# Performance work log

Hardware: AMD Instinct MI355X
Metric: run time of the kernel (lower is better)

## Reference

```python
import jax, jax.numpy as jnp
import numpy as np
from jax import lax

EPS = 1e-8


def _moving_average(x, window):
    # x: [B, T]; replicate-pad left by window-1, then mean-filter (matches F.pad(mode='replicate') + conv1d)
    pad = jnp.repeat(x[:, :1], window - 1, axis=1)
    xp = jnp.concatenate([pad, x], axis=1)[:, None, :]          # [B, 1, T+w-1]
    k = (jnp.ones((1, 1, window), x.dtype) / window)
    out = lax.conv_general_dilated(xp, k, (1,), 'VALID')         # [B, 1, T]
    return out[:, 0, :]


def _ema(x, period):
    # linear recurrence ema[t] = a*x[t] + (1-a)*ema[t-1], ema[0] = x[0]
    alpha = 2.0 / (period + 1)
    def step(carry, xt):
        y = alpha * xt + (1.0 - alpha) * carry
        return y, y
    init = x[:, 0]
    _, ys = lax.scan(step, init, x[:, 1:].T)                     # ys: [T-1, B]
    return jnp.concatenate([x[:, :1], ys.T], axis=1)


def _rsi(close, period=14):
    delta = jnp.diff(close, axis=1, prepend=close[:, :1])
    gain = jnp.where(delta > 0, delta, 0.0)
    loss = jnp.where(delta < 0, -delta, 0.0)
    avg_gain = _moving_average(gain, period)
    avg_loss = _moving_average(loss, period)
    rs = avg_gain / (avg_loss + EPS)
    return 100.0 - 100.0 / (1.0 + rs)


def _macd(close, fast=12, slow=26, signal=9):
    ema_fast = _ema(close, fast)
    ema_slow = _ema(close, slow)
    macd = ema_fast - ema_slow
    signal_line = _ema(macd, signal)
    return macd, signal_line


def _bollinger(close, period=20, num_std=2.0):
    ma = _moving_average(close, period)
    mean = _moving_average(close, period)
    sq_diff = (close - mean) ** 2
    variance = _moving_average(sq_diff, period)
    std = jnp.sqrt(variance + EPS)
    return ma + num_std * std, ma, ma - num_std * std


def _atr(close, period=14):
    high_low = jnp.abs(jnp.diff(close, axis=1, prepend=close[:, :1]))
    return _moving_average(high_low, period)


def _forward(close, volume):
    outs = []
    for window in (5, 10, 20, 50):
        ma = _moving_average(close, window)
        outs.append(ma)
        outs.append(close / (ma + EPS))
    outs.append(_rsi(close, 14))
    macd, signal = _macd(close)
    outs.append(macd)
    outs.append(signal)
    outs.append(macd - signal)
    bb_u, bb_m, bb_l = _bollinger(close, 20)
    outs.append(bb_u)
    outs.append(bb_m)
    outs.append(bb_l)
    outs.append((close - bb_l) / (bb_u - bb_l + EPS))
    outs.append(_atr(close, 14))
    return jnp.stack(outs)                                        # [17, B, T]


def setup_inputs() -> dict:
    key = jax.random.key(0)
    k1, k2 = jax.random.split(key)
    B, T = 512, 8192
    close = jax.random.uniform(k1, (B, T), dtype=jnp.float32)
    volume = jax.random.uniform(k2, (B, T), dtype=jnp.float32)
    return {"close": close, "volume": volume}


def reference(close, volume):
    return _forward(close, volume)
```

## Files before the change

### kernel.cpp

```cpp
#include <hip/hip_runtime.h>
#include <cstddef>

#define NTHREADS 256
#define TROW 8192
#define NROWS 512
#define TILE 1024
#define HALO 256
#define REG 1280
#define CHUNK 5
#define KOUT 4
#define FEPS 1e-8f

static_assert(REG == TILE + HALO, "region");
static_assert(CHUNK * NTHREADS == REG, "chunk");
static_assert(KOUT * NTHREADS == TILE, "kout");

__device__ __forceinline__ float pow_chunk(float b) {
  float b2 = b * b;
  return b2 * b2 * b;
}

template <typename SRC>
__device__ __forceinline__ void block_prefix(SRC src, float* __restrict__ dst,
                                             int tid, int lane, int wid,
                                             float* __restrict__ sc) {
  const int c0 = tid * CHUNK;
  float tot = 0.f;
#pragma unroll
  for (int k = 0; k < CHUNK; ++k) tot += src(c0 + k);
  float x = tot;
#pragma unroll
  for (int off = 1; off < 64; off <<= 1) {
    float y = __shfl_up(x, off, 64);
    if (lane >= off) x += y;
  }
  if (lane == 63) sc[wid] = x;
  __syncthreads();
  float woff = 0.f;
  for (int w = 0; w < wid; ++w) woff += sc[w];
  float run = woff + x - tot;
  if (tid == 0) dst[0] = 0.f;
#pragma unroll
  for (int k = 0; k < CHUNK; ++k) { run += src(c0 + k); dst[c0 + k + 1] = run; }
  __syncthreads();
}

__global__ __launch_bounds__(NTHREADS) void feat_kernel(
    const float* __restrict__ close, float* __restrict__ out) {
  __shared__ float cl[REG];
  __shared__ float Qa[REG + 1];
  __shared__ float Qb[REG + 1];
  __shared__ float sc[16];

  const int tid = threadIdx.x;
  const int lane = tid & 63;
  const int wid = tid >> 6;
  const int j = blockIdx.x;
  const int r = blockIdx.y;
  const int out_start = j * TILE;
  const int s = (j == 0) ? 0 : (out_start - HALO);
  const int ob = out_start - s;
  const size_t BT = (size_t)NROWS * TROW;
  const size_t rbase = (size_t)r * TROW + (size_t)s;

  const float* rp = close + rbase;
#pragma unroll
  for (int k = 0; k < CHUNK; ++k) {
    int i = tid + k * NTHREADS;
    cl[i] = rp[i];
  }
  __syncthreads();
  const float c0v = cl[0];

  block_prefix([&](int i) { return cl[i]; }, Qa, tid, lane, wid, sc);

#pragma unroll
  for (int k = 0; k < KOUT; ++k) {
    const int i = ob + tid + k * NTHREADS;
    const size_t base = rbase + (size_t)i;
    const float c = cl[i];
    const float q1 = Qa[i + 1];
#pragma unroll
    for (int wi = 0; wi < 4; ++wi) {
      const int w = (wi == 0) ? 5 : (wi == 1) ? 10 : (wi == 2) ? 20 : 50;
      const float invw = 1.f / (float)w;
      int al = i + 1 - w;
      float pad = 0.f;
      if (al < 0) { pad = (float)(-al) * c0v; al = 0; }
      const float ma = (q1 - Qa[al] + pad) * invw;
      out[(size_t)(2 * wi) * BT + base] = ma;
      out[(size_t)(2 * wi + 1) * BT + base] = c / (ma + FEPS);
    }
  }

  const bool first = (j == 0);
  block_prefix(
      [&](int i) -> float {
        if (!first && i < 19) return 0.f;
        int al = i - 19;
        float pad = 0.f;
        if (al < 0) { pad = (float)(-al) * c0v; al = 0; }
        const float m = (Qa[i + 1] - Qa[al] + pad) * 0.05f;
        const float d = cl[i] - m;
        return d * d;
      },
      Qb, tid, lane, wid, sc);

#pragma unroll
  for (int k = 0; k < KOUT; ++k) {
    const int i = ob + tid + k * NTHREADS;
    const size_t base = rbase + (size_t)i;
    const float c = cl[i];
    int al = i - 19;
    float pad = 0.f;
    if (al < 0) { pad = (float)(-al) * c0v; al = 0; }
    const float ma20 = (Qa[i + 1] - Qa[al] + pad) * 0.05f;
    int av = i - 19;
    if (av < 0) av = 0;
    float vs = Qb[i + 1] - Qb[av];
    vs = fmaxf(vs, 0.f);
    const float sd = sqrtf(vs * 0.05f + FEPS);
    const float up = ma20 + 2.f * sd;
    const float lo = ma20 - 2.f * sd;
    out[12 * BT + base] = up;
    out[13 * BT + base] = ma20;
    out[14 * BT + base] = lo;
    out[15 * BT + base] = (c - lo) / (up - lo + FEPS);
  }
  __syncthreads();

  block_prefix(
      [&](int i) -> float { return (i == 0) ? 0.f : fabsf(cl[i] - cl[i - 1]); },
      Qa, tid, lane, wid, sc);

#pragma unroll
  for (int k = 0; k < KOUT; ++k) {
    const int i = ob + tid + k * NTHREADS;
    const size_t base = rbase + (size_t)i;
    const float c = cl[i];
    int ar = i - 13;
    if (ar < 0) ar = 0;
    int ap = ar - 1;
    if (ap < 0) ap = 0;
    const float sabs = Qa[i + 1] - Qa[ar];
    const float sdel = c - cl[ap];
    const float g = (sabs + sdel) * (0.5f / 14.f);
    const float l = (sabs - sdel) * (0.5f / 14.f);
    const float rs = g / (l + FEPS);
    out[8 * BT + base] = 100.f - 100.f / (1.f + rs);
    out[16 * BT + base] = sabs * (1.f / 14.f);
  }

  {
    const float a12 = 2.f / 13.f, b12 = 11.f / 13.f;
    const float a26 = 2.f / 27.f, b26 = 25.f / 27.f;
    const int c0 = tid * CHUNK;
    float y1 = 0.f, y2 = 0.f;
#pragma unroll
    for (int k = 0; k < CHUNK; ++k) {
      const float x = cl[c0 + k];
      if (c0 + k == 0) { y1 = x; y2 = x; }
      else {
        y1 = fmaf(b12, y1, a12 * x);
        y2 = fmaf(b26, y2, a26 * x);
      }
    }
    float A1 = (tid == 0) ? 0.f : pow_chunk(b12);
    float A2 = (tid == 0) ? 0.f : pow_chunk(b26);
    float B1 = y1, B2 = y2;
#pragma unroll
    for (int off = 1; off < 64; off <<= 1) {
      const float pA1 = __shfl_up(A1, off, 64), pB1 = __shfl_up(B1, off, 64);
      const float pA2 = __shfl_up(A2, off, 64), pB2 = __shfl_up(B2, off, 64);
      if (lane >= off) {
        B1 = fmaf(A1, pB1, B1); A1 *= pA1;
        B2 = fmaf(A2, pB2, B2); A2 *= pA2;
      }
    }
    float eA1 = __shfl_up(A1, 1, 64), eB1 = __shfl_up(B1, 1, 64);
    float eA2 = __shfl_up(A2, 1, 64), eB2 = __shfl_up(B2, 1, 64);
    if (lane == 0) { eA1 = 1.f; eB1 = 0.f; eA2 = 1.f; eB2 = 0.f; }
    if (lane == 63) {
      sc[wid * 4 + 0] = A1; sc[wid * 4 + 1] = B1;
      sc[wid * 4 + 2] = A2; sc[wid * 4 + 3] = B2;
    }
    __syncthreads();
    float cB1 = 0.f, cB2 = 0.f;
    for (int w = 0; w < wid; ++w) {
      cB1 = fmaf(sc[w * 4 + 0], cB1, sc[w * 4 + 1]);
      cB2 = fmaf(sc[w * 4 + 2], cB2, sc[w * 4 + 3]);
    }
    y1 = fmaf(eA1, cB1, eB1);
    y2 = fmaf(eA2, cB2, eB2);
#pragma unroll
    for (int k = 0; k < CHUNK; ++k) {
      const float x = cl[c0 + k];
      if (c0 + k == 0) { y1 = x; y2 = x; }
      else {
        y1 = fmaf(b12, y1, a12 * x);
        y2 = fmaf(b26, y2, a26 * x);
      }
      Qb[c0 + k] = y1 - y2;
    }
    __syncthreads();
  }

  {
    const float a9 = 0.2f, b9 = 0.8f;
    const int c0 = tid * CHUNK;
    float y = 0.f;
#pragma unroll
    for (int k = 0; k < CHUNK; ++k) {
      const float x = Qb[c0 + k];
      if (c0 + k == 0) y = x;
      else y = fmaf(b9, y, a9 * x);
    }
    float A = (tid == 0) ? 0.f : pow_chunk(b9);
    float Bv = y;
#pragma unroll
    for (int off = 1; off < 64; off <<= 1) {
      const float pA = __shfl_up(A, off, 64), pB = __shfl_up(Bv, off, 64);
      if (lane >= off) { Bv = fmaf(A, pB, Bv); A *= pA; }
    }
    float eA = __shfl_up(A, 1, 64), eB = __shfl_up(Bv, 1, 64);
    if (lane == 0) { eA = 1.f; eB = 0.f; }
    if (lane == 63) { sc[wid * 2] = A; sc[wid * 2 + 1] = Bv; }
    __syncthreads();
    float cB = 0.f;
    for (int w = 0; w < wid; ++w) cB = fmaf(sc[w * 2], cB, sc[w * 2 + 1]);
    y = fmaf(eA, cB, eB);
#pragma unroll
    for (int k = 0; k < CHUNK; ++k) {
      const float x = Qb[c0 + k];
      if (c0 + k == 0) y = x;
      else y = fmaf(b9, y, a9 * x);
      Qa[c0 + k] = y;
    }
    __syncthreads();
  }

#pragma unroll
  for (int k = 0; k < KOUT; ++k) {
    const int i = ob + tid + k * NTHREADS;
    const size_t base = rbase + (size_t)i;
    const float m = Qb[i];
    const float sg = Qa[i];
    out[9 * BT + base] = m;
    out[10 * BT + base] = sg;
    out[11 * BT + base] = m - sg;
  }
}

extern "C" void kernel_launch(void* const* d_in, const int* in_sizes, int n_in,
                              void* d_out, int out_size, void* d_ws, size_t ws_size,
                              hipStream_t stream) {
  (void)in_sizes; (void)n_in; (void)out_size; (void)d_ws; (void)ws_size;
  const float* close = (const float*)d_in[0];
  float* out = (float*)d_out;
  dim3 grid(TROW / TILE, NROWS, 1);
  feat_kernel<<<grid, dim3(NTHREADS, 1, 1), 0, stream>>>(close, out);
}
```

Measured before the change: 303.0 us.

## Fuse prefix scans, pad shared buffers, and merge all output writes into one pass

Left-pads the shared arrays with replicate values so window lookups no longer need clamping or pad arithmetic, and loads input with float4. The squared-deviation and abs-delta prefix sums now run in one fused scan, which removes a block-wide scan and its barriers. All 17 outputs are written in a single final loop. Divisions and sqrt are replaced with hardware approximate rcp/sqrt builtins, and RSI is rewritten algebraically. Extra shared arrays raise LDS use per block, and the approximate intrinsics can change numerics slightly.

```diff
diff --git a/kernel.cpp b/kernel.cpp
--- a/kernel.cpp
+++ b/kernel.cpp
@@ -9,48 +9,26 @@
 #define REG 1280
 #define CHUNK 5
 #define KOUT 4
+#define PADL 64
 #define FEPS 1e-8f
 
 static_assert(REG == TILE + HALO, "region");
 static_assert(CHUNK * NTHREADS == REG, "chunk");
 static_assert(KOUT * NTHREADS == TILE, "kout");
 
-__device__ __forceinline__ float pow_chunk(float b) {
-  float b2 = b * b;
-  return b2 * b2 * b;
-}
-
-template <typename SRC>
-__device__ __forceinline__ void block_prefix(SRC src, float* __restrict__ dst,
-                                             int tid, int lane, int wid,
-                                             float* __restrict__ sc) {
-  const int c0 = tid * CHUNK;
-  float tot = 0.f;
-#pragma unroll
-  for (int k = 0; k < CHUNK; ++k) tot += src(c0 + k);
-  float x = tot;
-#pragma unroll
-  for (int off = 1; off < 64; off <<= 1) {
-    float y = __shfl_up(x, off, 64);
-    if (lane >= off) x += y;
-  }
-  if (lane == 63) sc[wid] = x;
-  __syncthreads();
-  float woff = 0.f;
-  for (int w = 0; w < wid; ++w) woff += sc[w];
-  float run = woff + x - tot;
-  if (tid == 0) dst[0] = 0.f;
-#pragma unroll
-  for (int k = 0; k < CHUNK; ++k) { run += src(c0 + k); dst[c0 + k + 1] = run; }
-  __syncthreads();
-}
+__device__ __forceinline__ float rcp_fast(float x) { return __builtin_amdgcn_rcpf(x); }
+__device__ __forceinline__ float sqrt_fast(float x) { return __builtin_amdgcn_sqrtf(x); }
+__device__ __forceinline__ float pow5(float b) { float b2 = b * b; return b2 * b2 * b; }
 
 __global__ __launch_bounds__(NTHREADS) void feat_kernel(
     const float* __restrict__ close, float* __restrict__ out) {
-  __shared__ float cl[REG];
-  __shared__ float Qa[REG + 1];
-  __shared__ float Qb[REG + 1];
-  __shared__ float sc[16];
+  __shared__ alignas(16) float cl[PADL + REG];
+  __shared__ float Qa[PADL + REG + 1];
+  __shared__ float Qs[PADL + REG + 1];
+  __shared__ float Qd[PADL + REG + 1];
+  __shared__ float Mm[REG];
+  __shared__ float Ss[REG];
+  __shared__ float sc[64];
 
   const int tid = threadIdx.x;
   const int lane = tid & 63;
@@ -63,110 +41,90 @@
   const size_t BT = (size_t)NROWS * TROW;
   const size_t rbase = (size_t)r * TROW + (size_t)s;
 
-  const float* rp = close + rbase;
-#pragma unroll
-  for (int k = 0; k < CHUNK; ++k) {
-    int i = tid + k * NTHREADS;
-    cl[i] = rp[i];
+  const float4* rp4 = (const float4*)(close + rbase);
+  ((float4*)(cl + PADL))[tid] = rp4[tid];
+  if (tid < (REG / 4 - NTHREADS))
+    ((float4*)(cl + PADL))[NTHREADS + tid] = rp4[NTHREADS + tid];
+  const float c0v = close[rbase];
+  if (tid < PADL) {
+    cl[tid] = c0v;
+    Qa[tid] = (float)(tid - PADL) * c0v;
+    Qs[tid] = 0.f;
+    Qd[tid] = 0.f;
   }
   __syncthreads();
-  const float c0v = cl[0];
-
-  block_prefix([&](int i) { return cl[i]; }, Qa, tid, lane, wid, sc);
-
-#pragma unroll
-  for (int k = 0; k < KOUT; ++k) {
-    const int i = ob + tid + k * NTHREADS;
-    const size_t base = rbase + (size_t)i;
-    const float c = cl[i];
-    const float q1 = Qa[i + 1];
-#pragma unroll
-    for (int wi = 0; wi < 4; ++wi) {
-      const int w = (wi == 0) ? 5 : (wi == 1) ? 10 : (wi == 2) ? 20 : 50;
-      const float invw = 1.f / (float)w;
-      int al = i + 1 - w;
-      float pad = 0.f;
-      if (al < 0) { pad = (float)(-al) * c0v; al = 0; }
-      const float ma = (q1 - Qa[al] + pad) * invw;
-      out[(size_t)(2 * wi) * BT + base] = ma;
-      out[(size_t)(2 * wi + 1) * BT + base] = c / (ma + FEPS);
-    }
-  }
-
-  const bool first = (j == 0);
-  block_prefix(
-      [&](int i) -> float {
-        if (!first && i < 19) return 0.f;
-        int al = i - 19;
-        float pad = 0.f;
-        if (al < 0) { pad = (float)(-al) * c0v; al = 0; }
-        const float m = (Qa[i + 1] - Qa[al] + pad) * 0.05f;
-        const float d = cl[i] - m;
-        return d * d;
-      },
-      Qb, tid, lane, wid, sc);
-
-#pragma unroll
-  for (int k = 0; k < KOUT; ++k) {
-    const int i = ob + tid + k * NTHREADS;
-    const size_t base = rbase + (size_t)i;
-    const float c = cl[i];
-    int al = i - 19;
-    float pad = 0.f;
-    if (al < 0) { pad = (float)(-al) * c0v; al = 0; }
-    const float ma20 = (Qa[i + 1] - Qa[al] + pad) * 0.05f;
-    int av = i - 19;
-    if (av < 0) av = 0;
-    float vs = Qb[i + 1] - Qb[av];
-    vs = fmaxf(vs, 0.f);
-    const float sd = sqrtf(vs * 0.05f + FEPS);
-    const float up = ma20 + 2.f * sd;
-    const float lo = ma20 - 2.f * sd;
-    out[12 * BT + base] = up;
-    out[13 * BT + base] = ma20;
-    out[14 * BT + base] = lo;
-    out[15 * BT + base] = (c - lo) / (up - lo + FEPS);
-  }
-  __syncthreads();
-
-  block_prefix(
-      [&](int i) -> float { return (i == 0) ? 0.f : fabsf(cl[i] - cl[i - 1]); },
-      Qa, tid, lane, wid, sc);
-
-#pragma unroll
-  for (int k = 0; k < KOUT; ++k) {
-    const int i = ob + tid + k * NTHREADS;
-    const size_t base = rbase + (size_t)i;
-    const float c = cl[i];
-    int ar = i - 13;
-    if (ar < 0) ar = 0;
-    int ap = ar - 1;
-    if (ap < 0) ap = 0;
-    const float sabs = Qa[i + 1] - Qa[ar];
-    const float sdel = c - cl[ap];
-    const float g = (sabs + sdel) * (0.5f / 14.f);
-    const float l = (sabs - sdel) * (0.5f / 14.f);
-    const float rs = g / (l + FEPS);
-    out[8 * BT + base] = 100.f - 100.f / (1.f + rs);
-    out[16 * BT + base] = sabs * (1.f / 14.f);
+
+  {
+    const int c0 = tid * CHUNK;
+    float v[CHUNK];
+    float tot = 0.f;
+#pragma unroll
+    for (int k = 0; k < CHUNK; ++k) { v[k] = cl[PADL + c0 + k]; tot += v[k]; }
+    float x = tot;
+#pragma unroll
+    for (int off = 1; off < 64; off <<= 1) {
+      float y = __shfl_up(x, off, 64);
+      if (lane >= off) x += y;
+    }
+    if (lane == 63) sc[wid] = x;
+    __syncthreads();
+    float run = x - tot;
+    for (int w = 0; w < wid; ++w) run += sc[w];
+    if (tid == 0) Qa[PADL] = 0.f;
+#pragma unroll
+    for (int k = 0; k < CHUNK; ++k) { run += v[k]; Qa[PADL + c0 + k + 1] = run; }
+    __syncthreads();
+  }
+
+  {
+    const int c0 = tid * CHUNK;
+    float a[CHUNK], b[CHUNK];
+    float t1 = 0.f, t2 = 0.f;
+#pragma unroll
+    for (int k = 0; k < CHUNK; ++k) {
+      const int p = PADL + c0 + k;
+      const float c = cl[p];
+      const float m20 = (Qa[p + 1] - Qa[p - 19]) * 0.05f;
+      const float d = c - m20;
+      a[k] = d * d; t1 += a[k];
+      b[k] = fabsf(c - cl[p - 1]); t2 += b[k];
+    }
+    float x1 = t1, x2 = t2;
+#pragma unroll
+    for (int off = 1; off < 64; off <<= 1) {
+      float y1 = __shfl_up(x1, off, 64);
+      float y2 = __shfl_up(x2, off, 64);
+      if (lane >= off) { x1 += y1; x2 += y2; }
+    }
+    if (lane == 63) { sc[8 + wid * 2] = x1; sc[8 + wid * 2 + 1] = x2; }
+    __syncthreads();
+    float r1 = x1 - t1, r2 = x2 - t2;
+    for (int w = 0; w < wid; ++w) { r1 += sc[8 + w * 2]; r2 += sc[8 + w * 2 + 1]; }
+    if (tid == 0) { Qs[PADL] = 0.f; Qd[PADL] = 0.f; }
+#pragma unroll
+    for (int k = 0; k < CHUNK; ++k) {
+      r1 += a[k]; Qs[PADL + c0 + k + 1] = r1;
+      r2 += b[k]; Qd[PADL + c0 + k + 1] = r2;
+    }
+    __syncthreads();
   }
 
   {
     const float a12 = 2.f / 13.f, b12 = 11.f / 13.f;
     const float a26 = 2.f / 27.f, b26 = 25.f / 27.f;
     const int c0 = tid * CHUNK;
+    float v[CHUNK];
+#pragma unroll
+    for (int k = 0; k < CHUNK; ++k) v[k] = cl[PADL + c0 + k];
     float y1 = 0.f, y2 = 0.f;
 #pragma unroll
     for (int k = 0; k < CHUNK; ++k) {
-      const float x = cl[c0 + k];
+      const float x = v[k];
       if (c0 + k == 0) { y1 = x; y2 = x; }
-      else {
-        y1 = fmaf(b12, y1, a12 * x);
-        y2 = fmaf(b26, y2, a26 * x);
-      }
-    }
-    float A1 = (tid == 0) ? 0.f : pow_chunk(b12);
-    float A2 = (tid == 0) ? 0.f : pow_chunk(b26);
+      else { y1 = fmaf(b12, y1, a12 * x); y2 = fmaf(b26, y2, a26 * x); }
+    }
+    float A1 = (tid == 0) ? 0.f : pow5(b12);
+    float A2 = (tid == 0) ? 0.f : pow5(b26);
     float B1 = y1, B2 = y2;
 #pragma unroll
     for (int off = 1; off < 64; off <<= 1) {
@@ -181,26 +139,23 @@
     float eA2 = __shfl_up(A2, 1, 64), eB2 = __shfl_up(B2, 1, 64);
     if (lane == 0) { eA1 = 1.f; eB1 = 0.f; eA2 = 1.f; eB2 = 0.f; }
     if (lane == 63) {
-      sc[wid * 4 + 0] = A1; sc[wid * 4 + 1] = B1;
-      sc[wid * 4 + 2] = A2; sc[wid * 4 + 3] = B2;
+      sc[16 + wid * 4 + 0] = A1; sc[16 + wid * 4 + 1] = B1;
+      sc[16 + wid * 4 + 2] = A2; sc[16 + wid * 4 + 3] = B2;
     }
     __syncthreads();
     float cB1 = 0.f, cB2 = 0.f;
     for (int w = 0; w < wid; ++w) {
-      cB1 = fmaf(sc[w * 4 + 0], cB1, sc[w * 4 + 1]);
-      cB2 = fmaf(sc[w * 4 + 2], cB2, sc[w * 4 + 3]);
+      cB1 = fmaf(sc[16 + w * 4 + 0], cB1, sc[16 + w * 4 + 1]);
+      cB2 = fmaf(sc[16 + w * 4 + 2], cB2, sc[16 + w * 4 + 3]);
     }
     y1 = fmaf(eA1, cB1, eB1);
     y2 = fmaf(eA2, cB2, eB2);
 #pragma unroll
     for (int k = 0; k < CHUNK; ++k) {
-      const float x = cl[c0 + k];
+      const float x = v[k];
       if (c0 + k == 0) { y1 = x; y2 = x; }
-      else {
-        y1 = fmaf(b12, y1, a12 * x);
-        y2 = fmaf(b26, y2, a26 * x);
-      }
-      Qb[c0 + k] = y1 - y2;
+      else { y1 = fmaf(b12, y1, a12 * x); y2 = fmaf(b26, y2, a26 * x); }
+      Mm[c0 + k] = y1 - y2;
     }
     __syncthreads();
   }
@@ -208,14 +163,17 @@
   {
     const float a9 = 0.2f, b9 = 0.8f;
     const int c0 = tid * CHUNK;
+    float v[CHUNK];
+#pragma unroll
+    for (int k = 0; k < CHUNK; ++k) v[k] = Mm[c0 + k];
     float y = 0.f;
 #pragma unroll
     for (int k = 0; k < CHUNK; ++k) {
-      const float x = Qb[c0 + k];
+      const float x = v[k];
       if (c0 + k == 0) y = x;
       else y = fmaf(b9, y, a9 * x);
     }
-    float A = (tid == 0) ? 0.f : pow_chunk(b9);
+    float A = (tid == 0) ? 0.f : pow5(b9);
     float Bv = y;
 #pragma unroll
     for (int off = 1; off < 64; off <<= 1) {
@@ -224,17 +182,17 @@
     }
     float eA = __shfl_up(A, 1, 64), eB = __shfl_up(Bv, 1, 64);
     if (lane == 0) { eA = 1.f; eB = 0.f; }
-    if (lane == 63) { sc[wid * 2] = A; sc[wid * 2 + 1] = Bv; }
+    if (lane == 63) { sc[40 + wid * 2] = A; sc[40 + wid * 2 + 1] = Bv; }
     __syncthreads();
     float cB = 0.f;
-    for (int w = 0; w < wid; ++w) cB = fmaf(sc[w * 2], cB, sc[w * 2 + 1]);
+    for (int w = 0; w < wid; ++w) cB = fmaf(sc[40 + w * 2], cB, sc[40 + w * 2 + 1]);
     y = fmaf(eA, cB, eB);
 #pragma unroll
     for (int k = 0; k < CHUNK; ++k) {
-      const float x = Qb[c0 + k];
+      const float x = v[k];
       if (c0 + k == 0) y = x;
       else y = fmaf(b9, y, a9 * x);
-      Qa[c0 + k] = y;
+      Ss[c0 + k] = y;
     }
     __syncthreads();
   }
@@ -242,12 +200,37 @@
 #pragma unroll
   for (int k = 0; k < KOUT; ++k) {
     const int i = ob + tid + k * NTHREADS;
-    const size_t base = rbase + (size_t)i;
-    const float m = Qb[i];
-    const float sg = Qa[i];
-    out[9 * BT + base] = m;
-    out[10 * BT + base] = sg;
-    out[11 * BT + base] = m - sg;
+    const int p = PADL + i;
+    float* o = out + (rbase + (size_t)i);
+    const float c = cl[p];
+    const float q1 = Qa[p + 1];
+    const float ma5  = (q1 - Qa[p - 4])  * 0.2f;
+    const float ma10 = (q1 - Qa[p - 9])  * 0.1f;
+    const float ma20 = (q1 - Qa[p - 19]) * 0.05f;
+    const float ma50 = (q1 - Qa[p - 49]) * 0.02f;
+    o[0]        = ma5;
+    o[1 * BT]   = c * rcp_fast(ma5 + FEPS);
+    o[2 * BT]   = ma10;
+    o[3 * BT]   = c * rcp_fast(ma10 + FEPS);
+    o[4 * BT]   = ma20;
+    o[5 * BT]   = c * rcp_fast(ma20 + FEPS);
+    o[6 * BT]   = ma50;
+    o[7 * BT]   = c * rcp_fast(ma50 + FEPS);
+    const float sabs = Qd[p + 1] - Qd[p - 13];
+    const float sdel = c - cl[p - 14];
+    o[8 * BT]   = 100.f * (sabs + sdel) * rcp_fast(2.f * sabs + 28.f * FEPS);
+    const float m = Mm[i], sg = Ss[i];
+    o[9 * BT]   = m;
+    o[10 * BT]  = sg;
+    o[11 * BT]  = m - sg;
+    const float var = fmaxf((Qs[p + 1] - Qs[p - 19]) * 0.05f, 0.f);
+    const float sd2 = 2.f * sqrt_fast(var + FEPS);
+    const float up = ma20 + sd2, lo = ma20 - sd2;
+    o[12 * BT]  = up;
+    o[13 * BT]  = ma20;
+    o[14 * BT]  = lo;
+    o[15 * BT]  = (c - lo) * rcp_fast(up - lo + FEPS);
+    o[16 * BT]  = sabs * (1.f / 14.f);
   }
 }
 
```

Measured after the change: 308.7 us. No clear change (+1.9%).
